# Optimization experiments

Measured on AMD Instinct MI355X. Metric: run time of the kernel, lower is better.

## Reference

```python
import jax, jax.numpy as jnp
import numpy as np
import math

B, SEQ_IN, D_IN = 4, 1028, 64
D = 1024          # hidden_size
H = 16            # num_heads
HD = D // H       # head_dim
L = 4             # num_layers
D_OUT = 1
EPS = 1e-6


def setup_inputs() -> dict:
    key = jax.random.key(0)
    ks = iter(jax.random.split(key, 32))
    s = 0.02
    inp = {}
    inp['x'] = jax.random.normal(next(ks), (B, SEQ_IN, D_IN), jnp.float32)
    # conv frontend (torch Conv1d weight layout: [out_ch, in_ch, k])
    inp['conv1_w'] = jax.random.normal(next(ks), (D // 2, D_IN, 3), jnp.float32) * s
    inp['conv1_b'] = jnp.zeros((D // 2,), jnp.float32)
    inp['conv2_w'] = jax.random.normal(next(ks), (D, D // 2, 3), jnp.float32) * s
    inp['conv2_b'] = jnp.zeros((D,), jnp.float32)
    # stacked per-layer params [L, ...]
    inp['lnA_w'] = jnp.ones((L, D), jnp.float32)
    inp['lnA_b'] = jnp.zeros((L, D), jnp.float32)
    inp['q_w'] = jax.random.normal(next(ks), (L, D, D), jnp.float32) * s
    inp['q_b'] = jnp.zeros((L, D), jnp.float32)
    inp['k_w'] = jax.random.normal(next(ks), (L, D, D), jnp.float32) * s
    inp['k_b'] = jnp.zeros((L, D), jnp.float32)
    inp['v_w'] = jax.random.normal(next(ks), (L, D, D), jnp.float32) * s
    inp['v_b'] = jnp.zeros((L, D), jnp.float32)
    inp['o_w'] = jax.random.normal(next(ks), (L, D, D), jnp.float32) * s
    inp['o_b'] = jnp.zeros((L, D), jnp.float32)
    inp['lnB_w'] = jnp.ones((L, D), jnp.float32)
    inp['lnB_b'] = jnp.zeros((L, D), jnp.float32)
    inp['f1_w'] = jax.random.normal(next(ks), (L, 2 * D, D), jnp.float32) * s
    inp['f1_b'] = jnp.zeros((L, 2 * D), jnp.float32)
    inp['f2_w'] = jax.random.normal(next(ks), (L, D, 2 * D), jnp.float32) * s
    inp['f2_b'] = jnp.zeros((L, D), jnp.float32)
    inp['fc_w'] = jax.random.normal(next(ks), (D_OUT, D), jnp.float32) * s
    inp['fc_b'] = jnp.zeros((D_OUT,), jnp.float32)
    return inp


def _layernorm(x, w, b):
    # torch-style: unbiased std (ddof=1), eps added to std (not var)
    mean = jnp.mean(x, axis=-1, keepdims=True)
    var = jnp.sum((x - mean) ** 2, axis=-1, keepdims=True) / (x.shape[-1] - 1)
    return w * ((x - mean) / (jnp.sqrt(var) + EPS)) + b


def _pos_encoding(S, d):
    pos = jnp.arange(S, dtype=jnp.float32)[:, None]
    div = jnp.exp(jnp.arange(0, d, 2, dtype=jnp.float32) * (-math.log(10000.0) / d))
    pe = jnp.zeros((S, d), jnp.float32)
    pe = pe.at[:, 0::2].set(jnp.sin(pos * div))
    pe = pe.at[:, 1::2].set(jnp.cos(pos * div))
    return pe


def _forward(x, conv1_w, conv1_b, conv2_w, conv2_b,
             lnA_w, lnA_b, q_w, q_b, k_w, k_b, v_w, v_b, o_w, o_b,
             lnB_w, lnB_b, f1_w, f1_b, f2_w, f2_b, fc_w, fc_b):
    dn = ('NCH', 'OIH', 'NCH')
    h = jnp.transpose(x, (0, 2, 1))                       # [B, D_in, S_in]
    h = jax.lax.conv_general_dilated(h, conv1_w, (1,), 'VALID', dimension_numbers=dn) + conv1_b[None, :, None]
    h = jax.lax.conv_general_dilated(h, conv2_w, (1,), 'VALID', dimension_numbers=dn) + conv2_b[None, :, None]
    h = jnp.transpose(h, (0, 2, 1))                       # [B, S, D]
    S = h.shape[1]
    h = h + _pos_encoding(S, D)[None]
    scale = 1.0 / math.sqrt(HD)

    def layer(xc, p):
        (lnaw, lnab, qw, qb, kw, kb, vw, vb, ow, ob,
         lnbw, lnbb, f1w, f1b, f2w, f2b) = p
        hn = _layernorm(xc, lnaw, lnab)
        q = (hn @ qw.T + qb).reshape(B, S, H, HD).transpose(0, 2, 1, 3)
        k = (hn @ kw.T + kb).reshape(B, S, H, HD).transpose(0, 2, 1, 3)
        v = (hn @ vw.T + vb).reshape(B, S, H, HD).transpose(0, 2, 1, 3)
        scores = jnp.einsum('bhsd,bhtd->bhst', q, k) * scale
        attn = scores / (1.0 + jnp.abs(scores))           # softsign, NOT softmax
        wv = jnp.einsum('bhst,bhtd->bhsd', attn, v)
        wv = wv.transpose(0, 2, 1, 3).reshape(B, S, D)
        xc = xc + (wv @ ow.T + ob)
        hn2 = _layernorm(xc, lnbw, lnbb)
        ff = jax.nn.relu(hn2 @ f1w.T + f1b) @ f2w.T + f2b
        return xc + ff, None

    params = (lnA_w, lnA_b, q_w, q_b, k_w, k_b, v_w, v_b, o_w, o_b,
              lnB_w, lnB_b, f1_w, f1_b, f2_w, f2_b)
    h, _ = jax.lax.scan(layer, h, params)
    pooled = jnp.mean(h, axis=1)                          # [B, D]
    return pooled @ fc_w.T + fc_b                         # [B, D_OUT]


def reference(x, conv1_w, conv1_b, conv2_w, conv2_b,
              lnA_w, lnA_b, q_w, q_b, k_w, k_b, v_w, v_b, o_w, o_b,
              lnB_w, lnB_b, f1_w, f1_b, f2_w, f2_b, fc_w, fc_b):
    return _forward(x, conv1_w, conv1_b, conv2_w, conv2_b,
                    lnA_w, lnA_b, q_w, q_b, k_w, k_b, v_w, v_b, o_w, o_b,
                    lnB_w, lnB_b, f1_w, f1_b, f2_w, f2_b, fc_w, fc_b)
```

## Files before the change

### kernel.cpp

```cpp
#include <hip/hip_runtime.h>
#include <hip/hip_bf16.h>
#include <math.h>

typedef __bf16 v8bf __attribute__((ext_vector_type(8)));
typedef float  v4f  __attribute__((ext_vector_type(4)));
typedef unsigned short v8us __attribute__((ext_vector_type(8)));

__device__ __forceinline__ unsigned short f2bfu(float f) {
    unsigned u = __builtin_bit_cast(unsigned, f);
    unsigned r = (u + 0x7fffu + ((u >> 16) & 1u)) >> 16;
    return (unsigned short)r;
}
__device__ __forceinline__ float bf2f(unsigned short u) {
    unsigned x = ((unsigned)u) << 16;
    return __builtin_bit_cast(float, x);
}

__device__ __forceinline__ long long swidx(int r, int k, int kt ) {
    return ((long long)((r >> 4) * kt + (k >> 5)) << 9)
         + (((k >> 3) & 3) << 7) + ((r & 15) << 3) + (k & 7);
}

#define GLDS16(g, s)                                                        \
    __builtin_amdgcn_global_load_lds(                                       \
        (const __attribute__((address_space(1))) void*)(g),                 \
        (__attribute__((address_space(3))) void*)(s), 16, 0, 0)

__global__ __launch_bounds__(256) void gemm_sw_k(
    const unsigned short* __restrict__ Asw,
    const unsigned short* __restrict__ Bsw,
    const float* __restrict__ bias,
    const float* __restrict__ res,
    float* __restrict__ Cf,
    unsigned short* __restrict__ Cb,
    unsigned short* __restrict__ Csw,
    unsigned short* __restrict__ Ct, int ctcol0,
    int M, int N, int K, int ldC, int relu)
{
    const int t = threadIdx.x;
    const int w = t >> 6;
    const int l = t & 63;

    int bx = blockIdx.x, by = blockIdx.y;
    {
        int nbx = gridDim.x;
        int nb  = nbx * gridDim.y;
        if ((nb & 7) == 0) {
            int bid = by * nbx + bx;
            int nid = (bid & 7) * (nb >> 3) + (bid >> 3);
            by = nid / nbx;
            bx = nid - by * nbx;
        }
    }
    const int m0 = by * 128;
    const int n0 = bx * 128;
    const int r16 = l & 15;
    const int qb  = l >> 4;
    const int wm = w >> 1, wn = w & 1;
    const int kt = K >> 5;

    const unsigned short* pa[4];
#pragma unroll
    for (int i = 0; i < 4; i++)
        pa[i] = Asw + ((long long)(((m0 >> 4) + 4 * wm + i) * kt) << 9) + l * 8;
    const unsigned short* pb[4];
#pragma unroll
    for (int j = 0; j < 4; j++)
        pb[j] = Bsw + ((long long)(((n0 >> 4) + 4 * wn + j) * kt) << 9) + l * 8;

    v4f acc[4][4];
#pragma unroll
    for (int i = 0; i < 4; i++)
#pragma unroll
        for (int j = 0; j < 4; j++) acc[i][j] = (v4f){0.f, 0.f, 0.f, 0.f};

    v8bf A0[4], A1[4], B0[4], B1[4];
#pragma unroll
    for (int i = 0; i < 4; i++) A0[i] = *(const v8bf*)(pa[i]);
#pragma unroll
    for (int j = 0; j < 4; j++) B0[j] = *(const v8bf*)(pb[j]);

    for (int s = 0; s < kt; s += 2) {
        {
            const long long o = (long long)(s + 1) << 9;
#pragma unroll
            for (int i = 0; i < 4; i++) A1[i] = *(const v8bf*)(pa[i] + o);
#pragma unroll
            for (int j = 0; j < 4; j++) B1[j] = *(const v8bf*)(pb[j] + o);
        }
#pragma unroll
        for (int i = 0; i < 4; i++)
#pragma unroll
            for (int j = 0; j < 4; j++)
                acc[i][j] = __builtin_amdgcn_mfma_f32_16x16x32_bf16(
                    A0[i], B0[j], acc[i][j], 0, 0, 0);
        if (s + 2 < kt) {
            const long long o = (long long)(s + 2) << 9;
#pragma unroll
            for (int i = 0; i < 4; i++) A0[i] = *(const v8bf*)(pa[i] + o);
#pragma unroll
            for (int j = 0; j < 4; j++) B0[j] = *(const v8bf*)(pb[j] + o);
        }
#pragma unroll
        for (int i = 0; i < 4; i++)
#pragma unroll
            for (int j = 0; j < 4; j++)
                acc[i][j] = __builtin_amdgcn_mfma_f32_16x16x32_bf16(
                    A1[i], B1[j], acc[i][j], 0, 0, 0);
    }

    float bv[4];
#pragma unroll
    for (int j = 0; j < 4; j++) bv[j] = bias[n0 + 64 * wn + 16 * j + r16];
    const int colbase = n0 + 64 * wn + r16;
    const int nt = N >> 5;
#pragma unroll
    for (int i = 0; i < 4; i++) {
        int rowb = m0 + 64 * wm + 16 * i + qb * 4;
#pragma unroll
        for (int j = 0; j < 4; j++) {
            int col = colbase + 16 * j;
            float v[4];
#pragma unroll
            for (int r = 0; r < 4; r++) v[r] = acc[i][j][r] + bv[j];
            if (Ct && col >= ctcol0) {
                ushort4 o;
                o.x = f2bfu(v[0]); o.y = f2bfu(v[1]);
                o.z = f2bfu(v[2]); o.w = f2bfu(v[3]);
                *(ushort4*)(Ct + ((long long)(rowb >> 10) << 20)
                            + (long long)(col - ctcol0) * 1024 + (rowb & 1023)) = o;
            } else if (Csw) {
#pragma unroll
                for (int r = 0; r < 4; r++) {
                    int row = rowb + r;
                    float vv = v[r];
                    if (relu) vv = fmaxf(vv, 0.f);
                    Csw[swidx(row, col, nt)] = f2bfu(vv);
                }
            } else {
#pragma unroll
                for (int r = 0; r < 4; r++) {
                    int row = rowb + r;
                    long long off = (long long)row * ldC + col;
                    float vv = v[r];
                    if (res)  vv += res[off];
                    if (relu) vv = fmaxf(vv, 0.f);
                    if (Cf) Cf[off] = vv;
                    if (Cb) ((unsigned short*)Cb)[off] = f2bfu(vv);
                }
            }
        }
    }
}

__global__ __launch_bounds__(256) void gemm_mfma_k(
    const __hip_bfloat16* __restrict__ A, int rpbA, long long bstrideA, int ldA,
    const __hip_bfloat16* __restrict__ B,
    const float* __restrict__ bias,
    const float* __restrict__ res,
    float* __restrict__ Cf,
    __hip_bfloat16* __restrict__ Cb,
    int M, int N, int K, int ldC, int relu)
{
    __shared__ __align__(16) __hip_bfloat16 As[2][8][64][8];
    __shared__ __align__(16) __hip_bfloat16 Bs[2][4][64][8];
    const int t  = threadIdx.x;
    const int w  = t >> 6;
    const int l  = t & 63;
    const int m0 = blockIdx.y * 128;
    const int n0 = blockIdx.x * 64;
    const int r16 = l & 15;
    const int qb  = l >> 4;
    const int wm = w >> 1, wn = w & 1;

    const __hip_bfloat16* gA[2];
#pragma unroll
    for (int tt = 0; tt < 2; tt++) {
        int arow = m0 + 16 * (2 * w + tt) + r16;
        gA[tt] = A + (long long)(arow / rpbA) * bstrideA
                   + (long long)(arow % rpbA) * ldA + qb * 8;
    }
    const __hip_bfloat16* gB = B + (long long)(n0 + 16 * w + r16) * K + qb * 8;

    v4f acc[4][2];
#pragma unroll
    for (int i = 0; i < 4; i++)
#pragma unroll
        for (int j = 0; j < 2; j++) acc[i][j] = (v4f){0.f, 0.f, 0.f, 0.f};

    GLDS16(gA[0], &As[0][2 * w + 0][0][0]);
    GLDS16(gA[1], &As[0][2 * w + 1][0][0]);
    GLDS16(gB,    &Bs[0][w][0][0]);
    __syncthreads();

    int cur = 0;
    for (int k0 = 32; k0 < K; k0 += 32) {
        v8bf af[4], bfr[2];
#pragma unroll
        for (int i = 0; i < 4; i++) af[i]  = *(const v8bf*)(&As[cur][4 * wm + i][l][0]);
#pragma unroll
        for (int j = 0; j < 2; j++) bfr[j] = *(const v8bf*)(&Bs[cur][2 * wn + j][l][0]);
        GLDS16(gA[0] + k0, &As[cur ^ 1][2 * w + 0][0][0]);
        GLDS16(gA[1] + k0, &As[cur ^ 1][2 * w + 1][0][0]);
        GLDS16(gB + k0,    &Bs[cur ^ 1][w][0][0]);
#pragma unroll
        for (int i = 0; i < 4; i++)
#pragma unroll
            for (int j = 0; j < 2; j++)
                acc[i][j] = __builtin_amdgcn_mfma_f32_16x16x32_bf16(
                    af[i], bfr[j], acc[i][j], 0, 0, 0);
        __syncthreads();
        cur ^= 1;
    }
    {
        v8bf af[4], bfr[2];
#pragma unroll
        for (int i = 0; i < 4; i++) af[i]  = *(const v8bf*)(&As[cur][4 * wm + i][l][0]);
#pragma unroll
        for (int j = 0; j < 2; j++) bfr[j] = *(const v8bf*)(&Bs[cur][2 * wn + j][l][0]);
#pragma unroll
        for (int i = 0; i < 4; i++)
#pragma unroll
            for (int j = 0; j < 2; j++)
                acc[i][j] = __builtin_amdgcn_mfma_f32_16x16x32_bf16(
                    af[i], bfr[j], acc[i][j], 0, 0, 0);
    }

    float bv[2];
#pragma unroll
    for (int j = 0; j < 2; j++) bv[j] = bias[n0 + 32 * wn + 16 * j + r16];
    const int colbase = n0 + 32 * wn + r16;
#pragma unroll
    for (int i = 0; i < 4; i++) {
        int rowb = m0 + 64 * wm + 16 * i + qb * 4;
#pragma unroll
        for (int j = 0; j < 2; j++) {
            int col = colbase + 16 * j;
#pragma unroll
            for (int r = 0; r < 4; r++) {
                int row = rowb + r;
                if (row >= M) continue;
                long long off = (long long)row * ldC + col;
                float vv = acc[i][j][r] + bv[j];
                if (res)  vv += res[off];
                if (relu) vv = fmaxf(vv, 0.f);
                if (Cf) Cf[off] = vv;
                if (Cb) ((unsigned short*)Cb)[off] = f2bfu(vv);
            }
        }
    }
}

__global__ __launch_bounds__(256) void attn_mfma_k(
    const unsigned short* __restrict__ QKV,
    const unsigned short* __restrict__ Vt,
    unsigned short* __restrict__ Osw)
{
    __shared__ __align__(16) unsigned short lds[25600];
    const int t = threadIdx.x, w = t >> 6, l = t & 63;
    const int bh = blockIdx.y, b = bh >> 4, h = bh & 15;
    const int s0 = blockIdx.x << 7;
    const int r16 = l & 15, q4 = l >> 4;
    const long long qrow0 = (long long)(b << 10) + s0;
    const int hoff = h << 6;

#pragma unroll
    for (int mi = 0; mi < 2; mi++)
#pragma unroll
        for (int kk = 0; kk < 2; kk++) {
            const unsigned short* g = QKV + (qrow0 + 32 * w + 16 * mi + r16) * 3072
                                      + hoff + 32 * kk + q4 * 8;
            GLDS16(g, &lds[(w * 4 + mi * 2 + kk) * 512]);
        }
    __syncthreads();
    v8bf qf[2][2];
#pragma unroll
    for (int mi = 0; mi < 2; mi++)
#pragma unroll
        for (int kk = 0; kk < 2; kk++)
            qf[mi][kk] = *(const v8bf*)&lds[(w * 4 + mi * 2 + kk) * 512 + l * 8];

    v4f oacc[2][4];
#pragma unroll
    for (int i = 0; i < 2; i++)
#pragma unroll
        for (int j = 0; j < 4; j++) oacc[i][j] = (v4f){0.f, 0.f, 0.f, 0.f};

    for (int t0 = 0; t0 < 1024; t0 += 64) {
#pragma unroll
        for (int rr = 0; rr < 2; rr++) {
            int r = 2 * w + rr, kk = r >> 2, j = r & 3;
            const unsigned short* gk = QKV
                + ((long long)(b << 10) + t0 + 16 * j + r16) * 3072
                + 1024 + hoff + 32 * kk + q4 * 8;
            GLDS16(gk, &lds[8192 + r * 512]);
            const unsigned short* gv = Vt + ((long long)b << 20)
                + (long long)(hoff + 16 * j + r16) * 1024 + t0 + 32 * kk + q4 * 8;
            GLDS16(gv, &lds[12288 + r * 512]);
        }
        __syncthreads();

        v8bf kf[2][4];
#pragma unroll
        for (int kk = 0; kk < 2; kk++)
#pragma unroll
            for (int j = 0; j < 4; j++)
                kf[kk][j] = *(const v8bf*)&lds[8192 + (kk * 4 + j) * 512 + l * 8];
        v4f sc[2][4];
#pragma unroll
        for (int i = 0; i < 2; i++)
#pragma unroll
            for (int j = 0; j < 4; j++) sc[i][j] = (v4f){0.f, 0.f, 0.f, 0.f};
#pragma unroll
        for (int kk = 0; kk < 2; kk++)
#pragma unroll
            for (int mi = 0; mi < 2; mi++)
#pragma unroll
                for (int j = 0; j < 4; j++)
                    sc[mi][j] = __builtin_amdgcn_mfma_f32_16x16x32_bf16(
                        qf[mi][kk], kf[kk][j], sc[mi][j], 0, 0, 0);

#pragma unroll
        for (int mi = 0; mi < 2; mi++)
#pragma unroll
            for (int j = 0; j < 4; j++)
#pragma unroll
                for (int r = 0; r < 4; r++) {
                    float v = sc[mi][j][r] * 0.125f;
                    float p = v * __builtin_amdgcn_rcpf(1.0f + fabsf(v));
                    lds[16384 + (32 * w + 16 * mi + q4 * 4 + r) * 72 + 16 * j + r16] = f2bfu(p);
                }

        v8bf pf[2][2], vf[2][4];
#pragma unroll
        for (int mi = 0; mi < 2; mi++)
#pragma unroll
            for (int kk = 0; kk < 2; kk++)
                pf[mi][kk] = *(const v8bf*)&lds[16384 + (32 * w + 16 * mi + r16) * 72
                                                + 32 * kk + q4 * 8];
#pragma unroll
        for (int kk = 0; kk < 2; kk++)
#pragma unroll
            for (int j = 0; j < 4; j++)
                vf[kk][j] = *(const v8bf*)&lds[12288 + (kk * 4 + j) * 512 + l * 8];
#pragma unroll
        for (int kk = 0; kk < 2; kk++)
#pragma unroll
            for (int mi = 0; mi < 2; mi++)
#pragma unroll
                for (int j = 0; j < 4; j++)
                    oacc[mi][j] = __builtin_amdgcn_mfma_f32_16x16x32_bf16(
                        pf[mi][kk], vf[kk][j], oacc[mi][j], 0, 0, 0);
        __syncthreads();
    }

#pragma unroll
    for (int mi = 0; mi < 2; mi++)
#pragma unroll
        for (int j = 0; j < 4; j++)
#pragma unroll
            for (int r = 0; r < 4; r++)
                lds[(32 * w + 16 * mi + q4 * 4 + r) * 72 + 16 * j + r16] =
                    f2bfu(oacc[mi][j][r]);
    __syncthreads();
    {
        int row = t >> 1, ch = (t & 1) << 5;
        int grow = (int)qrow0 + row;
#pragma unroll
        for (int i = 0; i < 4; i++) {
            int c0 = hoff + ch + 8 * i;
            v8us vv = *(const v8us*)&lds[row * 72 + ch + 8 * i];
            *(v8us*)(Osw + swidx(grow, c0, 32)) = vv;
        }
    }
}

__global__ __launch_bounds__(256) void layernorm_k(
    const float* __restrict__ x, const float* __restrict__ w,
    const float* __restrict__ b, unsigned short* __restrict__ ysw)
{
    int row = blockIdx.x;
    int t = threadIdx.x;
    float4 v = ((const float4*)(x + ((long long)row << 10)))[t];
    float s = v.x + v.y + v.z + v.w;
#pragma unroll
    for (int o = 32; o; o >>= 1) s += __shfl_down(s, o);
    __shared__ float red[4];
    __shared__ float red2[4];
    int wid = t >> 6, lane = t & 63;
    if (lane == 0) red[wid] = s;
    __syncthreads();
    float mean = (red[0] + red[1] + red[2] + red[3]) * (1.0f / 1024.0f);
    float dx = v.x - mean, dy = v.y - mean, dz = v.z - mean, dw = v.w - mean;
    float sq = dx * dx + dy * dy + dz * dz + dw * dw;
#pragma unroll
    for (int o = 32; o; o >>= 1) sq += __shfl_down(sq, o);
    if (lane == 0) red2[wid] = sq;
    __syncthreads();
    float var = (red2[0] + red2[1] + red2[2] + red2[3]) * (1.0f / 1023.0f);
    float inv = 1.0f / (sqrtf(var) + 1e-6f);
    float4 W  = ((const float4*)w)[t];
    float4 Bv = ((const float4*)b)[t];
    ushort4 o;
    o.x = f2bfu(W.x * (dx * inv) + Bv.x);
    o.y = f2bfu(W.y * (dy * inv) + Bv.y);
    o.z = f2bfu(W.z * (dz * inv) + Bv.z);
    o.w = f2bfu(W.w * (dw * inv) + Bv.w);
    int c0 = t << 2;
    *(ushort4*)(ysw + swidx(row, c0, 32)) = o;
}

__global__ __launch_bounds__(256) void add_pos_k(float* __restrict__ h)
{
    int idx = blockIdx.x * 256 + threadIdx.x;
    int d = idx & 1023;
    int s = (idx >> 10) & 1023;
    int e = d & ~1;
    float div = expf(-9.210340371976184f * (float)e * (1.0f / 1024.0f));
    float arg = (float)s * div;
    float pe = (d & 1) ? cosf(arg) : sinf(arg);
    h[idx] += pe;
}

__global__ __launch_bounds__(256) void convert_k(
    const float* __restrict__ src, unsigned short* __restrict__ dst, int n4)
{
    int i = blockIdx.x * 256 + threadIdx.x;
    if (i >= n4) return;
    float4 v = ((const float4*)src)[i];
    ushort4 o;
    o.x = f2bfu(v.x); o.y = f2bfu(v.y); o.z = f2bfu(v.z); o.w = f2bfu(v.w);
    ((ushort4*)dst)[i] = o;
}

__global__ __launch_bounds__(256) void convert_layer_sw_k(
    const float* __restrict__ q, const float* __restrict__ k,
    const float* __restrict__ v, const float* __restrict__ o,
    const float* __restrict__ f1, const float* __restrict__ f2,
    unsigned short* __restrict__ dst)
{
    int idx = blockIdx.x * 256 + threadIdx.x;
    const float* src;
    unsigned short* db;
    int Ksh, rf;
    if (idx < 0x100000) {
        int region = idx >> 18;
        rf = idx & 0x3FFFF;
        src = (region == 0) ? q : (region == 1) ? k : (region == 2) ? v : o;
        db = dst + ((long long)region << 20);
        Ksh = 10;
    } else if (idx < 0x180000) {
        rf = idx - 0x100000; src = f1; db = dst + (4LL << 20); Ksh = 10;
    } else {
        rf = idx - 0x180000; src = f2; db = dst + (6LL << 20); Ksh = 11;
    }
    float4 vv = ((const float4*)src)[rf];
    int flatf = rf << 2;
    int n  = flatf >> Ksh;
    int k0 = flatf & ((1 << Ksh) - 1);
    ushort4 ov;
    ov.x = f2bfu(vv.x); ov.y = f2bfu(vv.y); ov.z = f2bfu(vv.z); ov.w = f2bfu(vv.w);
    *(ushort4*)(db + swidx(n, k0, 1 << (Ksh - 5))) = ov;
}

__global__ __launch_bounds__(256) void concat3_k(
    const float* __restrict__ a, const float* __restrict__ b,
    const float* __restrict__ c, float* __restrict__ o)
{
    int i = blockIdx.x * 256 + threadIdx.x;
    o[i] = (i < 1024) ? a[i] : ((i < 2048) ? b[i - 1024] : c[i - 2048]);
}

__global__ __launch_bounds__(256) void reorder_w_k(
    const float* __restrict__ src, unsigned short* __restrict__ dst, int OC, int IC)
{
    int idx = blockIdx.x * 256 + threadIdx.x;
    if (idx >= OC * IC * 3) return;
    int k  = idx % 3;
    int ic = (idx / 3) % IC;
    int oc = idx / (3 * IC);
    dst[(oc * 3 + k) * IC + ic] = f2bfu(src[idx]);
}

__global__ __launch_bounds__(256) void meanpool_part_k(
    const float* __restrict__ h, float* __restrict__ part)
{
    int g = blockIdx.x;
    int b = g >> 6, rblk = g & 63;
    const float4* base = (const float4*)(h + ((long long)b << 20)
                                           + ((long long)(rblk * 16) << 10));
    float4 s = {0.f, 0.f, 0.f, 0.f};
#pragma unroll
    for (int i = 0; i < 16; i++) {
        float4 v = base[i * 256 + threadIdx.x];
        s.x += v.x; s.y += v.y; s.z += v.z; s.w += v.w;
    }
    ((float4*)part)[g * 256 + threadIdx.x] = s;
}

__global__ __launch_bounds__(256) void meanpool_red_k(
    const float* __restrict__ part, float* __restrict__ pooled)
{
    int idx = blockIdx.x * 256 + threadIdx.x;
    int b = idx >> 10, d = idx & 1023;
    const float* p = part + ((long long)(b * 64) << 10) + d;
    float s = 0.f;
#pragma unroll 8
    for (int r = 0; r < 64; r++) s += p[r << 10];
    pooled[idx] = s * (1.0f / 1024.0f);
}

__global__ __launch_bounds__(256) void fc_k(
    const float* __restrict__ p, const float* __restrict__ w,
    const float* __restrict__ fb, float* __restrict__ out)
{
    int b = blockIdx.x, t = threadIdx.x;
    float s = 0.f;
    for (int i = t; i < 1024; i += 256) s += p[(b << 10) + i] * w[i];
#pragma unroll
    for (int o = 32; o; o >>= 1) s += __shfl_down(s, o);
    __shared__ float red[4];
    if ((t & 63) == 0) red[t >> 6] = s;
    __syncthreads();
    if (t == 0) out[b] = red[0] + red[1] + red[2] + red[3] + fb[0];
}

extern "C" void kernel_launch(void* const* d_in, const int* in_sizes, int n_in,
                              void* d_out, int out_size, void* d_ws, size_t ws_size,
                              hipStream_t stream)
{
    const float* x    = (const float*)d_in[0];
    const float* c1w  = (const float*)d_in[1];
    const float* c1b  = (const float*)d_in[2];
    const float* c2w  = (const float*)d_in[3];
    const float* c2b  = (const float*)d_in[4];
    const float* lnAw = (const float*)d_in[5];
    const float* lnAb = (const float*)d_in[6];
    const float* qw   = (const float*)d_in[7];
    const float* qbi  = (const float*)d_in[8];
    const float* kw   = (const float*)d_in[9];
    const float* kbi  = (const float*)d_in[10];
    const float* vw   = (const float*)d_in[11];
    const float* vbi  = (const float*)d_in[12];
    const float* ow   = (const float*)d_in[13];
    const float* obi  = (const float*)d_in[14];
    const float* lnBw = (const float*)d_in[15];
    const float* lnBb = (const float*)d_in[16];
    const float* f1w  = (const float*)d_in[17];
    const float* f1b  = (const float*)d_in[18];
    const float* f2w  = (const float*)d_in[19];
    const float* f2b  = (const float*)d_in[20];
    const float* fcw  = (const float*)d_in[21];
    const float* fcb  = (const float*)d_in[22];
    float* out = (float*)d_out;

    float* ws = (float*)d_ws;
    typedef __hip_bfloat16 bf;
    typedef unsigned short us;
    float* h    = ws;
    us* hn_b    = (us*)(ws + 4194304);
    us* qkv_b   = (us*)(ws + 6291456);
    us* ff_b    = qkv_b;
    us* wq_b    = (us*)(ws + 12582912);
    us* wo_b    = (us*)(ws + 14155776);
    us* wf1_b   = (us*)(ws + 14680064);
    us* wf2_b   = (us*)(ws + 15728640);
    us* xb      = (us*)(ws + 16777216);
    us* h1b     = (us*)(ws + 16912896);
    us* w1t_b   = (us*)(ws + 17963520);
    us* w2t_b   = (us*)(ws + 18012672);
    float* pooled = ws + 18799104;
    us* Vt      = (us*)(ws + 18803200);
    float* bqkv = ws + 20900352;
    float* mp_part = ws + 20903424;

    convert_k<<<dim3(257), 256, 0, stream>>>(x, xb, 65792);
    reorder_w_k<<<dim3(384),  256, 0, stream>>>(c1w, w1t_b, 512, 64);
    reorder_w_k<<<dim3(6144), 256, 0, stream>>>(c2w, w2t_b, 1024, 512);

    gemm_mfma_k<<<dim3(8, 33), 256, 0, stream>>>(
        (const bf*)xb, 1026, 1028LL * 64, 64, (const bf*)w1t_b,
        c1b, nullptr, nullptr, (bf*)h1b, 4104, 512, 192, 512, 0);
    gemm_mfma_k<<<dim3(16, 32), 256, 0, stream>>>(
        (const bf*)h1b, 1024, 1026LL * 512, 512, (const bf*)w2t_b,
        c2b, nullptr, h, nullptr, 4096, 1024, 1536, 1024, 0);
    add_pos_k<<<dim3(16384), 256, 0, stream>>>(h);

    for (int l = 0; l < 4; l++) {
        long long wo  = (long long)l * 1048576;
        long long wo2 = (long long)l * 2097152;
        convert_layer_sw_k<<<dim3(8192), 256, 0, stream>>>(
            qw + wo, kw + wo, vw + wo, ow + wo, f1w + wo2, f2w + wo2, wq_b);
        concat3_k<<<dim3(12), 256, 0, stream>>>(qbi + l * 1024, kbi + l * 1024,
                                                vbi + l * 1024, bqkv);

        layernorm_k<<<dim3(4096), 256, 0, stream>>>(h, lnAw + l * 1024, lnAb + l * 1024, hn_b);
        gemm_sw_k<<<dim3(24, 32), 256, 0, stream>>>(
            hn_b, wq_b, bqkv, nullptr, nullptr, qkv_b, nullptr, Vt, 2048,
            4096, 3072, 1024, 3072, 0);
        attn_mfma_k<<<dim3(8, 64), 256, 0, stream>>>(qkv_b, Vt, hn_b);
        gemm_sw_k<<<dim3(8, 32), 256, 0, stream>>>(
            hn_b, wo_b, obi + l * 1024, h, h, nullptr, nullptr, nullptr, 0,
            4096, 1024, 1024, 1024, 0);
        layernorm_k<<<dim3(4096), 256, 0, stream>>>(h, lnBw + l * 1024, lnBb + l * 1024, hn_b);
        gemm_sw_k<<<dim3(16, 32), 256, 0, stream>>>(
            hn_b, wf1_b, f1b + l * 2048, nullptr, nullptr, nullptr, ff_b, nullptr, 0,
            4096, 2048, 1024, 2048, 1);
        gemm_sw_k<<<dim3(8, 32), 256, 0, stream>>>(
            ff_b, wf2_b, f2b + l * 1024, h, h, nullptr, nullptr, nullptr, 0,
            4096, 1024, 2048, 1024, 0);
    }

    meanpool_part_k<<<dim3(256), 256, 0, stream>>>(h, mp_part);
    meanpool_red_k<<<dim3(16), 256, 0, stream>>>(mp_part, pooled);
    fc_k<<<dim3(4), 256, 0, stream>>>(pooled, fcw, fcb, out);
}
```

Before: 1.164 ms.

## Split GEMM blocks into single-wave 64x64 tiles with 4-deep register prefetch

Each GEMM block now holds one wavefront that computes a 64x64 tile instead of four waves sharing a 128x128 tile, and the launch grids grow fourfold to match. The K loop switches from double buffering to a four-stage rotating register prefetch of the swizzled A/B fragments, hiding more global-load latency. Operands come straight from global memory, so smaller tiles mean less reuse per fetch and more total traffic. The deeper buffers also raise register pressure, which the launch bounds of 64 threads with a minimum of 2 blocks per multiprocessor must accommodate.

Result: no change. 1.143 ms (-1.8%).

```diff
diff --git a/kernel.cpp b/kernel.cpp
--- a/kernel.cpp
+++ b/kernel.cpp
@@ -26,7 +26,24 @@
         (const __attribute__((address_space(1))) void*)(g),                 \
         (__attribute__((address_space(3))) void*)(s), 16, 0, 0)
 
-__global__ __launch_bounds__(256) void gemm_sw_k(
+#define LOAD_CHUNK(R, C) do {                                               \
+    const long long o_ = (long long)(C) << 9;                               \
+    _Pragma("unroll")                                                       \
+    for (int i_ = 0; i_ < 4; i_++) Ab[R][i_] = *(const v8bf*)(pa[i_] + o_); \
+    _Pragma("unroll")                                                       \
+    for (int j_ = 0; j_ < 4; j_++) Bb[R][j_] = *(const v8bf*)(pb[j_] + o_); \
+} while (0)
+
+#define MFMA_CHUNK(R) do {                                                  \
+    _Pragma("unroll")                                                       \
+    for (int i_ = 0; i_ < 4; i_++)                                          \
+    _Pragma("unroll")                                                       \
+    for (int j_ = 0; j_ < 4; j_++)                                          \
+        acc[i_][j_] = __builtin_amdgcn_mfma_f32_16x16x32_bf16(              \
+            Ab[R][i_], Bb[R][j_], acc[i_][j_], 0, 0, 0);                    \
+} while (0)
+
+__global__ __launch_bounds__(64, 2) void gemm_sw_k(
     const unsigned short* __restrict__ Asw,
     const unsigned short* __restrict__ Bsw,
     const float* __restrict__ bias,
@@ -37,9 +54,7 @@
     unsigned short* __restrict__ Ct, int ctcol0,
     int M, int N, int K, int ldC, int relu)
 {
-    const int t = threadIdx.x;
-    const int w = t >> 6;
-    const int l = t & 63;
+    const int l = threadIdx.x;
 
     int bx = blockIdx.x, by = blockIdx.y;
     {
@@ -52,21 +67,20 @@
             bx = nid - by * nbx;
         }
     }
-    const int m0 = by * 128;
-    const int n0 = bx * 128;
+    const int m0 = by * 64;
+    const int n0 = bx * 64;
     const int r16 = l & 15;
     const int qb  = l >> 4;
-    const int wm = w >> 1, wn = w & 1;
     const int kt = K >> 5;
 
     const unsigned short* pa[4];
 #pragma unroll
     for (int i = 0; i < 4; i++)
-        pa[i] = Asw + ((long long)(((m0 >> 4) + 4 * wm + i) * kt) << 9) + l * 8;
+        pa[i] = Asw + ((long long)(((m0 >> 4) + i) * kt) << 9) + l * 8;
     const unsigned short* pb[4];
 #pragma unroll
     for (int j = 0; j < 4; j++)
-        pb[j] = Bsw + ((long long)(((n0 >> 4) + 4 * wn + j) * kt) << 9) + l * 8;
+        pb[j] = Bsw + ((long long)(((n0 >> 4) + j) * kt) << 9) + l * 8;
 
     v4f acc[4][4];
 #pragma unroll
@@ -74,49 +88,30 @@
 #pragma unroll
         for (int j = 0; j < 4; j++) acc[i][j] = (v4f){0.f, 0.f, 0.f, 0.f};
 
-    v8bf A0[4], A1[4], B0[4], B1[4];
-#pragma unroll
-    for (int i = 0; i < 4; i++) A0[i] = *(const v8bf*)(pa[i]);
-#pragma unroll
-    for (int j = 0; j < 4; j++) B0[j] = *(const v8bf*)(pb[j]);
-
-    for (int s = 0; s < kt; s += 2) {
-        {
-            const long long o = (long long)(s + 1) << 9;
-#pragma unroll
-            for (int i = 0; i < 4; i++) A1[i] = *(const v8bf*)(pa[i] + o);
-#pragma unroll
-            for (int j = 0; j < 4; j++) B1[j] = *(const v8bf*)(pb[j] + o);
-        }
-#pragma unroll
-        for (int i = 0; i < 4; i++)
-#pragma unroll
-            for (int j = 0; j < 4; j++)
-                acc[i][j] = __builtin_amdgcn_mfma_f32_16x16x32_bf16(
-                    A0[i], B0[j], acc[i][j], 0, 0, 0);
-        if (s + 2 < kt) {
-            const long long o = (long long)(s + 2) << 9;
-#pragma unroll
-            for (int i = 0; i < 4; i++) A0[i] = *(const v8bf*)(pa[i] + o);
-#pragma unroll
-            for (int j = 0; j < 4; j++) B0[j] = *(const v8bf*)(pb[j] + o);
-        }
-#pragma unroll
-        for (int i = 0; i < 4; i++)
-#pragma unroll
-            for (int j = 0; j < 4; j++)
-                acc[i][j] = __builtin_amdgcn_mfma_f32_16x16x32_bf16(
-                    A1[i], B1[j], acc[i][j], 0, 0, 0);
-    }
+    v8bf Ab[4][4], Bb[4][4];
+
+    LOAD_CHUNK(0, 0);
+    LOAD_CHUNK(1, 1);
+    LOAD_CHUNK(2, 2);
+
+    int s = 0;
+    for (; s < kt - 4; s += 4) {
+        LOAD_CHUNK(3, s + 3); MFMA_CHUNK(0);
+        LOAD_CHUNK(0, s + 4); MFMA_CHUNK(1);
+        LOAD_CHUNK(1, s + 5); MFMA_CHUNK(2);
+        LOAD_CHUNK(2, s + 6); MFMA_CHUNK(3);
+    }
+    LOAD_CHUNK(3, kt - 1);
+    MFMA_CHUNK(0); MFMA_CHUNK(1); MFMA_CHUNK(2); MFMA_CHUNK(3);
 
     float bv[4];
 #pragma unroll
-    for (int j = 0; j < 4; j++) bv[j] = bias[n0 + 64 * wn + 16 * j + r16];
-    const int colbase = n0 + 64 * wn + r16;
+    for (int j = 0; j < 4; j++) bv[j] = bias[n0 + 16 * j + r16];
+    const int colbase = n0 + r16;
     const int nt = N >> 5;
 #pragma unroll
     for (int i = 0; i < 4; i++) {
-        int rowb = m0 + 64 * wm + 16 * i + qb * 4;
+        int rowb = m0 + 16 * i + qb * 4;
 #pragma unroll
         for (int j = 0; j < 4; j++) {
             int col = colbase + 16 * j;
@@ -595,18 +590,18 @@
                                                 vbi + l * 1024, bqkv);
 
         layernorm_k<<<dim3(4096), 256, 0, stream>>>(h, lnAw + l * 1024, lnAb + l * 1024, hn_b);
-        gemm_sw_k<<<dim3(24, 32), 256, 0, stream>>>(
+        gemm_sw_k<<<dim3(48, 64), 64, 0, stream>>>(
             hn_b, wq_b, bqkv, nullptr, nullptr, qkv_b, nullptr, Vt, 2048,
             4096, 3072, 1024, 3072, 0);
         attn_mfma_k<<<dim3(8, 64), 256, 0, stream>>>(qkv_b, Vt, hn_b);
-        gemm_sw_k<<<dim3(8, 32), 256, 0, stream>>>(
+        gemm_sw_k<<<dim3(16, 64), 64, 0, stream>>>(
             hn_b, wo_b, obi + l * 1024, h, h, nullptr, nullptr, nullptr, 0,
             4096, 1024, 1024, 1024, 0);
         layernorm_k<<<dim3(4096), 256, 0, stream>>>(h, lnBw + l * 1024, lnBb + l * 1024, hn_b);
-        gemm_sw_k<<<dim3(16, 32), 256, 0, stream>>>(
+        gemm_sw_k<<<dim3(32, 64), 64, 0, stream>>>(
             hn_b, wf1_b, f1b + l * 2048, nullptr, nullptr, nullptr, ff_b, nullptr, 0,
             4096, 2048, 1024, 2048, 1);
-        gemm_sw_k<<<dim3(8, 32), 256, 0, stream>>>(
+        gemm_sw_k<<<dim3(16, 64), 64, 0, stream>>>(
             ff_b, wf2_b, f2b + l * 1024, h, h, nullptr, nullptr, nullptr, 0,
             4096, 1024, 2048, 1024, 0);
     }
```
